# Optimization experiments

Hardware: AMD Instinct MI355X
Metric: run time of the kernel (lower is better)

The kernel has to match this reference:

```python
import jax, jax.numpy as jnp
import numpy as np

AUX_LOSS_ALPHA = 0.01
TOP_K = 2
N_EXPERTS = 64


def setup_inputs() -> dict:
    key = jax.random.key(0)
    k1, k2 = jax.random.split(key)
    B, S, H, E = 4, 4096, 2048, N_EXPERTS
    hidden_states = jax.random.normal(k1, (B, S, H), dtype=jnp.float32)
    # kaiming_uniform_(a=sqrt(5)) ~ U(-1/sqrt(H), 1/sqrt(H))
    bound = 1.0 / np.sqrt(H)
    weight = jax.random.uniform(k2, (E, H), dtype=jnp.float32, minval=-bound, maxval=bound)
    return {"hidden_states": hidden_states, "weight": weight}


def reference(hidden_states, weight):
    B, S, H = hidden_states.shape
    E, K = N_EXPERTS, TOP_K
    x = hidden_states.reshape(-1, H)              # [T, H], T = B*S
    logits = jnp.einsum('th,eh->te', x, weight)   # router GEMM [T, E]
    scores = jax.nn.softmax(logits, axis=-1)
    topk_weight, topk_idx = jax.lax.top_k(scores, K)  # [T, K]
    # norm_topk_prob (K > 1)
    topk_weight = topk_weight / (jnp.sum(topk_weight, axis=-1, keepdims=True) + 1e-20)
    # seq_aux auxiliary loss (training path)
    idx2d = topk_idx.reshape(B, S * K)            # [B, S*K]
    ce = jnp.zeros((B, E), dtype=scores.dtype)
    ce = ce.at[jnp.arange(B)[:, None], idx2d].add(1.0)
    ce = ce / (S * K / E)
    scores3 = scores.reshape(B, S, E)
    aux_loss = jnp.mean(jnp.sum(ce * jnp.mean(scores3, axis=1), axis=1)) * AUX_LOSS_ALPHA
    return topk_idx, topk_weight, aux_loss
```

## Files before the change

### kernel.cpp

```cpp
#include <hip/hip_runtime.h>
#include <math.h>


#define TT 16384
#define HH 2048
#define EE 64
#define BB 4
#define M_TOK 16
#define KCH 256
#define TAU 2e-3f
#define NREP 8

typedef float v4f __attribute__((ext_vector_type(4)));
typedef float f4v __attribute__((ext_vector_type(4)));
typedef short s8v __attribute__((ext_vector_type(8)));

__device__ __forceinline__ unsigned short f2bf(float f) {
    unsigned u = __float_as_uint(f);
    return (unsigned short)((u + 0x7fffu + ((u >> 16) & 1u)) >> 16);
}
__device__ __forceinline__ float bf2f(unsigned short h) {
    return __uint_as_float(((unsigned)h) << 16);
}

__global__ void prep_b(const float* __restrict__ w,
                       unsigned short* __restrict__ bhi,
                       unsigned short* __restrict__ blo) {
    int idx = blockIdx.x * blockDim.x + threadIdx.x;
    int j    = idx & 7;
    int lane = (idx >> 3) & 63;
    int ks   = (idx >> 9) & 63;
    int nt   = idx >> 15;
    int e = nt * 16 + (lane & 15);
    int k = ks * 32 + (lane >> 4) * 8 + j;
    float f = w[e * HH + k];
    unsigned short h = f2bf(f);
    bhi[idx] = h;
    blo[idx] = f2bf(f - bf2f(h));
}

__global__ __launch_bounds__(256) void gemm_logits(
    const float* __restrict__ x,
    const unsigned short* __restrict__ bhi, const unsigned short* __restrict__ blo,
    float* __restrict__ logits) {

    __shared__ unsigned short ahi[2][8 * 64 * 8];
    __shared__ unsigned short alo[2][8 * 64 * 8];

    const int tid  = threadIdx.x;
    const int wave = tid >> 6;
    const int lane = tid & 63;
    const int tok0 = blockIdx.x * M_TOK;
    const int m  = tid >> 4;
    const int kb = tid & 15;

    v4f rx[2][4];

    auto LD = [&](int c, int s) {
        const float* __restrict__ xp = x + (size_t)(tok0 + m) * HH + c * KCH + kb * 8;
        rx[s][0] = *(const v4f*)xp;
        rx[s][1] = *(const v4f*)(xp + 4);
        rx[s][2] = *(const v4f*)(xp + 128);
        rx[s][3] = *(const v4f*)(xp + 132);
    };
    auto ST = [&](int s, int bi) {
#pragma unroll
        for (int g = 0; g < 2; ++g) {
            v4f a = rx[s][g * 2], b2 = rx[s][g * 2 + 1];
            float xs[8] = {a.x, a.y, a.z, a.w, b2.x, b2.y, b2.z, b2.w};
            s8v hv, lv;
#pragma unroll
            for (int j = 0; j < 8; ++j) {
                unsigned short h = f2bf(xs[j]);
                hv[j] = (short)h;
                lv[j] = (short)f2bf(xs[j] - bf2f(h));
            }
            const int k8i = kb + g * 16;
            const int kstep = k8i >> 2, quad = k8i & 3;
            const int entry = kstep * 64 + quad * 16 + (m ^ (quad << 1));
            *(s8v*)&ahi[bi][entry * 8] = hv;
            *(s8v*)&alo[bi][entry * 8] = lv;
        }
    };

    LD(0, 0);
    LD(1, 1);
    ST(0, 0);
    __syncthreads();

    f4v acc = {0.f, 0.f, 0.f, 0.f};
    const int rdl = lane ^ ((lane >> 4) << 1);

#pragma unroll
    for (int c = 0; c < 8; ++c) {
        const int cur = c & 1;
        if (c < 6) LD(c + 2, cur);
        if (c < 7) ST(cur ^ 1, cur ^ 1);
#pragma unroll
        for (int ks = 0; ks < 8; ++ks) {
            const int entry = ks * 64 + rdl;
            s8v af_h = *(const s8v*)&ahi[cur][entry * 8];
            s8v af_l = *(const s8v*)&alo[cur][entry * 8];
            const size_t boff = ((size_t)(wave * 64 + c * 8 + ks) * 64 + lane) * 8;
            s8v bf_h = *(const s8v*)&bhi[boff];
            s8v bf_l = *(const s8v*)&blo[boff];
            acc = __builtin_amdgcn_mfma_f32_16x16x32_bf16(af_h, bf_h, acc, 0, 0, 0);
            acc = __builtin_amdgcn_mfma_f32_16x16x32_bf16(af_h, bf_l, acc, 0, 0, 0);
            acc = __builtin_amdgcn_mfma_f32_16x16x32_bf16(af_l, bf_h, acc, 0, 0, 0);
        }
        __syncthreads();
    }

#pragma unroll
    for (int r = 0; r < 4; ++r)
        logits[(size_t)(tok0 + (lane >> 4) * 4 + r) * EE + wave * 16 + (lane & 15)] = acc[r];
}

__global__ __launch_bounds__(256) void gate_topk(
    const float* __restrict__ logits,
    float* __restrict__ out_idx, float* __restrict__ out_w,
    float* __restrict__ g_cnt, float* __restrict__ g_ssum,
    int* __restrict__ wl_cnt, int* __restrict__ wl) {

    __shared__ float bssum[EE];
    const int tid  = threadIdx.x;
    const int lane = tid & 63;
    const int t    = blockIdx.x * 4 + (tid >> 6);
    const int rep  = (blockIdx.x & (NREP - 1)) * (BB * EE);

    if (tid < EE) bssum[tid] = 0.f;

    float l = logits[(size_t)t * EE + lane];

    float mx = l;
#pragma unroll
    for (int off = 32; off; off >>= 1) mx = fmaxf(mx, __shfl_xor(mx, off, 64));
    float p = __expf(l - mx);
    float Z = p;
#pragma unroll
    for (int off = 32; off; off >>= 1) Z += __shfl_xor(Z, off, 64);
    float s = p / Z;

    float v = l;
    int cand[4]; float cl[4];
#pragma unroll
    for (int r = 0; r < 4; ++r) {
        float bv = v; int bi = lane;
#pragma unroll
        for (int off = 32; off; off >>= 1) {
            float ov = __shfl_xor(bv, off, 64);
            int   oi = __shfl_xor(bi, off, 64);
            if (ov > bv || (ov == bv && oi < bi)) { bv = ov; bi = oi; }
        }
        cand[r] = bi; cl[r] = bv;
        if (lane == bi) v = -3.4e38f;
    }

    __syncthreads();
    atomicAdd(&bssum[lane], s);

    if (lane == 0) {
        const int b = t >> 12;
        atomicAdd(&g_cnt[rep + b * EE + cand[0]], 1.f);
        atomicAdd(&g_cnt[rep + b * EE + cand[1]], 1.f);
        float w1 = 1.f / (1.f + __expf(cl[1] - cl[0]));
        out_idx[t * 2]     = (float)cand[0];
        out_idx[t * 2 + 1] = (float)cand[1];
        out_w[t * 2]       = w1;
        out_w[t * 2 + 1]   = 1.f - w1;
        if (cl[0] - cl[1] < TAU || cl[1] - cl[2] < TAU) {
            int pos = atomicAdd(wl_cnt, 1);
            wl[pos] = t;
        }
    }

    __syncthreads();
    if (tid < EE) {
        const int b0 = (blockIdx.x * 4) >> 12;
        atomicAdd(&g_ssum[rep + b0 * EE + tid], bssum[tid]);
    }
}

__global__ __launch_bounds__(256) void rerank_exact(
    const float* __restrict__ logits, const float* __restrict__ x,
    const float* __restrict__ w,
    const int* __restrict__ wl_cnt, const int* __restrict__ wl,
    float* __restrict__ out_idx, float* __restrict__ out_w) {

    const int lane = threadIdx.x & 63;
    const int wid  = blockIdx.x * 4 + (threadIdx.x >> 6);
    const int n    = wl_cnt[0];

    for (int i = wid; i < n; i += 32 * 4) {
        const int t = wl[i];
        float l = logits[(size_t)t * EE + lane];

        float v = l;
        int cand[4];
#pragma unroll
        for (int r = 0; r < 4; ++r) {
            float bv = v; int bi = lane;
#pragma unroll
            for (int off = 32; off; off >>= 1) {
                float ov = __shfl_xor(bv, off, 64);
                int   oi = __shfl_xor(bi, off, 64);
                if (ov > bv || (ov == bv && oi < bi)) { bv = ov; bi = oi; }
            }
            cand[r] = bi;
            if (lane == bi) v = -3.4e38f;
        }

        const float* __restrict__ xt  = x + (size_t)t * HH;
        const float* __restrict__ w0p = w + (size_t)cand[0] * HH;
        const float* __restrict__ w1p = w + (size_t)cand[1] * HH;
        const float* __restrict__ w2p = w + (size_t)cand[2] * HH;
        const float* __restrict__ w3p = w + (size_t)cand[3] * HH;
        double d0 = 0.0, d1 = 0.0, d2 = 0.0, d3 = 0.0;
#pragma unroll
        for (int ii = 0; ii < 8; ++ii) {
            const int k = ii * 256 + lane * 4;
            v4f xv = *(const v4f*)(xt + k);
            v4f a0 = *(const v4f*)(w0p + k);
            v4f a1 = *(const v4f*)(w1p + k);
            v4f a2 = *(const v4f*)(w2p + k);
            v4f a3 = *(const v4f*)(w3p + k);
            double dx0 = (double)xv.x, dx1 = (double)xv.y;
            double dx2 = (double)xv.z, dx3 = (double)xv.w;
            d0 = fma(dx0, (double)a0.x, d0); d0 = fma(dx1, (double)a0.y, d0);
            d0 = fma(dx2, (double)a0.z, d0); d0 = fma(dx3, (double)a0.w, d0);
            d1 = fma(dx0, (double)a1.x, d1); d1 = fma(dx1, (double)a1.y, d1);
            d1 = fma(dx2, (double)a1.z, d1); d1 = fma(dx3, (double)a1.w, d1);
            d2 = fma(dx0, (double)a2.x, d2); d2 = fma(dx1, (double)a2.y, d2);
            d2 = fma(dx2, (double)a2.z, d2); d2 = fma(dx3, (double)a2.w, d2);
            d3 = fma(dx0, (double)a3.x, d3); d3 = fma(dx1, (double)a3.y, d3);
            d3 = fma(dx2, (double)a3.z, d3); d3 = fma(dx3, (double)a3.w, d3);
        }
#pragma unroll
        for (int off = 32; off; off >>= 1) {
            d0 += __shfl_xor(d0, off, 64);
            d1 += __shfl_xor(d1, off, 64);
            d2 += __shfl_xor(d2, off, 64);
            d3 += __shfl_xor(d3, off, 64);
        }

        double bd[4] = {d0, d1, d2, d3};
        int e1 = cand[0]; double l1 = bd[0];
#pragma unroll
        for (int r = 1; r < 4; ++r)
            if (bd[r] > l1 || (bd[r] == l1 && cand[r] < e1)) { l1 = bd[r]; e1 = cand[r]; }
        int e2 = -1; double l2 = -1e300;
#pragma unroll
        for (int r = 0; r < 4; ++r) {
            if (cand[r] == e1) continue;
            if (e2 < 0 || bd[r] > l2 || (bd[r] == l2 && cand[r] < e2)) { l2 = bd[r]; e2 = cand[r]; }
        }

        double w1 = 1.0 / (1.0 + exp(l2 - l1));
        if (lane == 0) {
            out_idx[t * 2]     = (float)e1;
            out_idx[t * 2 + 1] = (float)e2;
            out_w[t * 2]       = (float)w1;
            out_w[t * 2 + 1]   = (float)(1.0 - w1);
        }
    }
}

__global__ void finalize(const float* __restrict__ g_cnt,
                         const float* __restrict__ g_ssum,
                         float* __restrict__ aux_out) {
    int lane = threadIdx.x;
    float a = 0.f;
    for (int b = 0; b < BB; ++b) {
        float c = 0.f, ss = 0.f;
#pragma unroll
        for (int r = 0; r < NREP; ++r) {
            c  += g_cnt[r * (BB * EE) + b * EE + lane];
            ss += g_ssum[r * (BB * EE) + b * EE + lane];
        }
        a += c * ss;
    }
#pragma unroll
    for (int off = 32; off; off >>= 1) a += __shfl_xor(a, off, 64);
    if (lane == 0) aux_out[0] = a * (0.01f / (4.f * 128.f * 4096.f));
}

extern "C" void kernel_launch(void* const* d_in, const int* in_sizes, int n_in,
                              void* d_out, int out_size, void* d_ws, size_t ws_size,
                              hipStream_t stream) {
    const float* x = (const float*)d_in[0];
    const float* w = (const float*)d_in[1];
    float* out = (float*)d_out;
    float* out_idx = out;
    float* out_w   = out + 2 * TT;
    float* aux     = out + 4 * TT;

    float* logits = (float*)d_ws;
    unsigned short* bhi = (unsigned short*)(logits + (size_t)TT * EE);
    unsigned short* blo = bhi + (size_t)EE * HH;
    float* g_cnt  = (float*)(blo + (size_t)EE * HH);
    float* g_ssum = g_cnt + NREP * BB * EE;
    int*   wl_cnt = (int*)(g_ssum + NREP * BB * EE);
    int*   wl     = wl_cnt + 16;

    hipMemsetAsync(g_cnt, 0, (2 * NREP * BB * EE + 16) * sizeof(float), stream);
    prep_b<<<(EE * HH) / 256, 256, 0, stream>>>(w, bhi, blo);
    gemm_logits<<<TT / M_TOK, 256, 0, stream>>>(x, bhi, blo, logits);
    gate_topk<<<TT / 4, 256, 0, stream>>>(logits, out_idx, out_w,
                                          g_cnt, g_ssum, wl_cnt, wl);
    rerank_exact<<<32, 256, 0, stream>>>(logits, x, w, wl_cnt, wl, out_idx, out_w);
    finalize<<<1, 64, 0, stream>>>(g_cnt, g_ssum, aux);
}
```

Before: 245.7 us.

## Fuse gating/top-k into GEMM epilogue and merge finalize into rerank

Softmax, top-k selection, load counting and score-sum accumulation move into the GEMM kernel's epilogue, which reads logits from shared memory. Logits are still written to global memory for the rerank pass. The separate memset becomes a zeroing step inside prep_b, and the finalize kernel becomes an extra block of the rerank kernel. This removes two to three launches and one global read of the logits, but finalize now runs alongside rerank instead of after it. Since rerank blocks do not write g_cnt or g_ssum, the ordering should still be correct.

New measurement: 231.1 us. 1.06x faster.

```diff
diff --git a/kernel.cpp b/kernel.cpp
--- a/kernel.cpp
+++ b/kernel.cpp
@@ -25,7 +25,11 @@
 
 __global__ void prep_b(const float* __restrict__ w,
                        unsigned short* __restrict__ bhi,
-                       unsigned short* __restrict__ blo) {
+                       unsigned short* __restrict__ blo,
+                       float* __restrict__ zreg) {
+    if (blockIdx.x == 0) {
+        for (int i = threadIdx.x; i < 2 * NREP * BB * EE + 16; i += 256) zreg[i] = 0.f;
+    }
     int idx = blockIdx.x * blockDim.x + threadIdx.x;
     int j    = idx & 7;
     int lane = (idx >> 3) & 63;
@@ -39,13 +43,18 @@
     blo[idx] = f2bf(f - bf2f(h));
 }
 
-__global__ __launch_bounds__(256) void gemm_logits(
+__global__ __launch_bounds__(256) void gemm_gate(
     const float* __restrict__ x,
     const unsigned short* __restrict__ bhi, const unsigned short* __restrict__ blo,
-    float* __restrict__ logits) {
+    float* __restrict__ logits,
+    float* __restrict__ out_idx, float* __restrict__ out_w,
+    float* __restrict__ g_cnt, float* __restrict__ g_ssum,
+    int* __restrict__ wl_cnt, int* __restrict__ wl) {
 
     __shared__ unsigned short ahi[2][8 * 64 * 8];
     __shared__ unsigned short alo[2][8 * 64 * 8];
+    __shared__ float lg[M_TOK][68];
+    __shared__ float bssum[EE];
 
     const int tid  = threadIdx.x;
     const int wave = tid >> 6;
@@ -53,6 +62,8 @@
     const int tok0 = blockIdx.x * M_TOK;
     const int m  = tid >> 4;
     const int kb = tid & 15;
+
+    if (tid < EE) bssum[tid] = 0.f;
 
     v4f rx[2][4];
 
@@ -112,80 +123,95 @@
     }
 
 #pragma unroll
-    for (int r = 0; r < 4; ++r)
-        logits[(size_t)(tok0 + (lane >> 4) * 4 + r) * EE + wave * 16 + (lane & 15)] = acc[r];
-}
-
-__global__ __launch_bounds__(256) void gate_topk(
-    const float* __restrict__ logits,
-    float* __restrict__ out_idx, float* __restrict__ out_w,
-    float* __restrict__ g_cnt, float* __restrict__ g_ssum,
-    int* __restrict__ wl_cnt, int* __restrict__ wl) {
-
-    __shared__ float bssum[EE];
-    const int tid  = threadIdx.x;
-    const int lane = tid & 63;
-    const int t    = blockIdx.x * 4 + (tid >> 6);
-    const int rep  = (blockIdx.x & (NREP - 1)) * (BB * EE);
-
-    if (tid < EE) bssum[tid] = 0.f;
-
-    float l = logits[(size_t)t * EE + lane];
-
-    float mx = l;
-#pragma unroll
-    for (int off = 32; off; off >>= 1) mx = fmaxf(mx, __shfl_xor(mx, off, 64));
-    float p = __expf(l - mx);
-    float Z = p;
-#pragma unroll
-    for (int off = 32; off; off >>= 1) Z += __shfl_xor(Z, off, 64);
-    float s = p / Z;
-
-    float v = l;
-    int cand[4]; float cl[4];
-#pragma unroll
     for (int r = 0; r < 4; ++r) {
-        float bv = v; int bi = lane;
-#pragma unroll
-        for (int off = 32; off; off >>= 1) {
-            float ov = __shfl_xor(bv, off, 64);
-            int   oi = __shfl_xor(bi, off, 64);
-            if (ov > bv || (ov == bv && oi < bi)) { bv = ov; bi = oi; }
-        }
-        cand[r] = bi; cl[r] = bv;
-        if (lane == bi) v = -3.4e38f;
-    }
-
+        const int row = (lane >> 4) * 4 + r;
+        const int col = wave * 16 + (lane & 15);
+        lg[row][col] = acc[r];
+        logits[(size_t)(tok0 + row) * EE + col] = acc[r];
+    }
     __syncthreads();
-    atomicAdd(&bssum[lane], s);
-
-    if (lane == 0) {
-        const int b = t >> 12;
-        atomicAdd(&g_cnt[rep + b * EE + cand[0]], 1.f);
-        atomicAdd(&g_cnt[rep + b * EE + cand[1]], 1.f);
-        float w1 = 1.f / (1.f + __expf(cl[1] - cl[0]));
-        out_idx[t * 2]     = (float)cand[0];
-        out_idx[t * 2 + 1] = (float)cand[1];
-        out_w[t * 2]       = w1;
-        out_w[t * 2 + 1]   = 1.f - w1;
-        if (cl[0] - cl[1] < TAU || cl[1] - cl[2] < TAU) {
-            int pos = atomicAdd(wl_cnt, 1);
-            wl[pos] = t;
-        }
-    }
-
+
+    const int b   = tok0 >> 12;
+    const int rep = (blockIdx.x & (NREP - 1)) * (BB * EE);
+    float ssum_l = 0.f;
+
+#pragma unroll
+    for (int r = 0; r < 4; ++r) {
+        const int tl = wave * 4 + r;
+        const int t  = tok0 + tl;
+        float l = lg[tl][lane];
+
+        float mx = l;
+#pragma unroll
+        for (int off = 32; off; off >>= 1) mx = fmaxf(mx, __shfl_xor(mx, off, 64));
+        float p = __expf(l - mx);
+        float Z = p;
+#pragma unroll
+        for (int off = 32; off; off >>= 1) Z += __shfl_xor(Z, off, 64);
+        ssum_l += p / Z;
+
+        float v = l;
+        int cand[3]; float cl[3];
+#pragma unroll
+        for (int q = 0; q < 3; ++q) {
+            float bv = v; int bi = lane;
+#pragma unroll
+            for (int off = 32; off; off >>= 1) {
+                float ov = __shfl_xor(bv, off, 64);
+                int   oi = __shfl_xor(bi, off, 64);
+                if (ov > bv || (ov == bv && oi < bi)) { bv = ov; bi = oi; }
+            }
+            cand[q] = bi; cl[q] = bv;
+            if (lane == bi) v = -3.4e38f;
+        }
+
+        if (lane == 0) {
+            atomicAdd(&g_cnt[rep + b * EE + cand[0]], 1.f);
+            atomicAdd(&g_cnt[rep + b * EE + cand[1]], 1.f);
+            float w1 = 1.f / (1.f + __expf(cl[1] - cl[0]));
+            out_idx[t * 2]     = (float)cand[0];
+            out_idx[t * 2 + 1] = (float)cand[1];
+            out_w[t * 2]       = w1;
+            out_w[t * 2 + 1]   = 1.f - w1;
+            if (cl[0] - cl[1] < TAU || cl[1] - cl[2] < TAU) {
+                int pos = atomicAdd(wl_cnt, 1);
+                wl[pos] = t;
+            }
+        }
+    }
+
+    atomicAdd(&bssum[lane], ssum_l);
     __syncthreads();
-    if (tid < EE) {
-        const int b0 = (blockIdx.x * 4) >> 12;
-        atomicAdd(&g_ssum[rep + b0 * EE + tid], bssum[tid]);
-    }
-}
-
-__global__ __launch_bounds__(256) void rerank_exact(
+    if (tid < EE) atomicAdd(&g_ssum[rep + b * EE + tid], bssum[tid]);
+}
+
+__global__ __launch_bounds__(256) void rerank_fin(
     const float* __restrict__ logits, const float* __restrict__ x,
     const float* __restrict__ w,
     const int* __restrict__ wl_cnt, const int* __restrict__ wl,
-    float* __restrict__ out_idx, float* __restrict__ out_w) {
+    float* __restrict__ out_idx, float* __restrict__ out_w,
+    const float* __restrict__ g_cnt, const float* __restrict__ g_ssum,
+    float* __restrict__ aux_out) {
+
+    if (blockIdx.x == 32) {
+        if (threadIdx.x < 64) {
+            int lane = threadIdx.x;
+            float a = 0.f;
+            for (int b = 0; b < BB; ++b) {
+                float c = 0.f, ss = 0.f;
+#pragma unroll
+                for (int rr = 0; rr < NREP; ++rr) {
+                    c  += g_cnt[rr * (BB * EE) + b * EE + lane];
+                    ss += g_ssum[rr * (BB * EE) + b * EE + lane];
+                }
+                a += c * ss;
+            }
+#pragma unroll
+            for (int off = 32; off; off >>= 1) a += __shfl_xor(a, off, 64);
+            if (lane == 0) aux_out[0] = a * (0.01f / (4.f * 128.f * 4096.f));
+        }
+        return;
+    }
 
     const int lane = threadIdx.x & 63;
     const int wid  = blockIdx.x * 4 + (threadIdx.x >> 6);
@@ -265,25 +291,6 @@
     }
 }
 
-__global__ void finalize(const float* __restrict__ g_cnt,
-                         const float* __restrict__ g_ssum,
-                         float* __restrict__ aux_out) {
-    int lane = threadIdx.x;
-    float a = 0.f;
-    for (int b = 0; b < BB; ++b) {
-        float c = 0.f, ss = 0.f;
-#pragma unroll
-        for (int r = 0; r < NREP; ++r) {
-            c  += g_cnt[r * (BB * EE) + b * EE + lane];
-            ss += g_ssum[r * (BB * EE) + b * EE + lane];
-        }
-        a += c * ss;
-    }
-#pragma unroll
-    for (int off = 32; off; off >>= 1) a += __shfl_xor(a, off, 64);
-    if (lane == 0) aux_out[0] = a * (0.01f / (4.f * 128.f * 4096.f));
-}
-
 extern "C" void kernel_launch(void* const* d_in, const int* in_sizes, int n_in,
                               void* d_out, int out_size, void* d_ws, size_t ws_size,
                               hipStream_t stream) {
@@ -302,11 +309,9 @@
     int*   wl_cnt = (int*)(g_ssum + NREP * BB * EE);
     int*   wl     = wl_cnt + 16;
 
-    hipMemsetAsync(g_cnt, 0, (2 * NREP * BB * EE + 16) * sizeof(float), stream);
-    prep_b<<<(EE * HH) / 256, 256, 0, stream>>>(w, bhi, blo);
-    gemm_logits<<<TT / M_TOK, 256, 0, stream>>>(x, bhi, blo, logits);
-    gate_topk<<<TT / 4, 256, 0, stream>>>(logits, out_idx, out_w,
-                                          g_cnt, g_ssum, wl_cnt, wl);
-    rerank_exact<<<32, 256, 0, stream>>>(logits, x, w, wl_cnt, wl, out_idx, out_w);
-    finalize<<<1, 64, 0, stream>>>(g_cnt, g_ssum, aux);
-}
+    prep_b<<<(EE * HH) / 256, 256, 0, stream>>>(w, bhi, blo, g_cnt);
+    gemm_gate<<<TT / M_TOK, 256, 0, stream>>>(x, bhi, blo, logits,
+                                              out_idx, out_w, g_cnt, g_ssum, wl_cnt, wl);
+    rerank_fin<<<33, 256, 0, stream>>>(logits, x, w, wl_cnt, wl,
+                                       out_idx, out_w, g_cnt, g_ssum, aux);
+}
```
